# Kernel tuning notes

Measured on AMD Instinct MI355X. Metric: run time of the kernel, lower is better.

Reference implementation:

```python
import jax, jax.numpy as jnp
import numpy as np

# Config (matches init_kwargs)
B, T, N = 32, 512, 1024
FT, FS = 16, 32                 # max_time_F, max_space_F
NCH = FT * FS                   # n_channels = 512
MULT = 2
DIN = NCH * MULT                # input_dim = 1024
H = 1024                        # hidden_size
NCLS = 1                        # n_cls_tokens
NP = (T // FT) * (N // FS)      # n_patches = 1024
SCALE = float(H) ** 0.5         # config.scale is None -> hidden_size**0.5


def setup_inputs() -> dict:
    key = jax.random.key(0)
    k0, k1, k2, k3 = jax.random.split(key, 4)
    s = 0.02
    return {
        "spikes": jax.random.normal(k0, (B, T, N), dtype=jnp.float32),
        "W_embed": jax.random.normal(k1, (DIN, NCH), dtype=jnp.float32) * s,
        "b_embed": jnp.zeros((DIN,), dtype=jnp.float32),
        "cls_tokens": jnp.zeros((1, NCLS, DIN), dtype=jnp.float32),
        "W_proj": jax.random.normal(k2, (H, DIN), dtype=jnp.float32) * s,
        "b_proj": jnp.zeros((H,), dtype=jnp.float32),
        "pos_table": jax.random.normal(k3, (NP + NCLS, H), dtype=jnp.float32) * s,
    }


def reference(spikes, W_embed, b_embed, cls_tokens, W_proj, b_proj, pos_table):
    Bsz = spikes.shape[0]
    # Patchify: replaces the double python loop with one reshape/transpose.
    # [B,T,N] -> [B, T/FT, FT, N/FS, FS] -> [B, T/FT, N/FS, FT, FS] -> [B, NP, NCH]
    # flatten order (time-major within patch) matches torch's .flatten(1) on [B,FT,FS].
    patches = spikes.reshape(Bsz, T // FT, FT, N // FS, FS)
    patches = patches.transpose(0, 1, 3, 2, 4).reshape(Bsz, NP, NCH)
    # embed_spikes (linear)
    x = jnp.einsum("bpc,dc->bpd", patches, W_embed) + b_embed
    # prepend cls tokens
    cls = jnp.broadcast_to(cls_tokens, (Bsz, NCLS, DIN))
    x = jnp.concatenate([cls, x], axis=1)
    # act * scale, then projection
    x = jax.nn.gelu(x, approximate=False) * SCALE
    x = jnp.einsum("bpd,hd->bph", x, W_proj) + b_proj
    # positional embedding: stamps are arange, so direct table add
    stamp = jnp.broadcast_to(
        jnp.arange(NP + NCLS, dtype=jnp.int32)[None, :], (Bsz, NP + NCLS)
    )
    mask = jnp.ones((Bsz, NP + NCLS), dtype=jnp.int32)
    x = x + pos_table[None, :, :]
    # dropout p=0.0 -> identity
    return (x, mask, stamp)
```

## Files before the change

kernel.cpp:

```cpp
#include <hip/hip_runtime.h>
#include <stdint.h>


typedef __attribute__((ext_vector_type(8))) short bf16x8;
typedef __attribute__((ext_vector_type(4))) float f32x4;

__device__ __forceinline__ unsigned short f2bf(float f) {
  union { float f; unsigned u; } v; v.f = f;
  const unsigned u = v.u;
  return (unsigned short)((u + 0x7fffu + ((u >> 16) & 1u)) >> 16);
}

__device__ __forceinline__ float gelu_exact(float x) {
  return 0.5f * x * (1.0f + erff(x * 0.70710678118654752440f));
}

__device__ __forceinline__ void gl_lds16(const unsigned short* g, unsigned short* l) {
  __builtin_amdgcn_global_load_lds(
      (const __attribute__((address_space(1))) unsigned int*)g,
      (__attribute__((address_space(3))) unsigned int*)l, 16, 0, 0);
}


__global__ void cast_f32_bf16(const float* __restrict__ src,
                              unsigned short* __restrict__ dst, int n) {
  const int i = blockIdx.x * 256 + threadIdx.x;
  if (i < n) dst[i] = f2bf(src[i]);
}

__global__ void patchify(const float* __restrict__ spikes,
                         unsigned short* __restrict__ P) {
  const int idx = blockIdx.x * 256 + threadIdx.x;
  const int m = idx >> 7;
  const int c = (idx & 127) << 2;
  const int b = m >> 10, p = m & 1023;
  const int pt = p >> 5, ps = p & 31;
  const int ft = c >> 5, fs = c & 31;
  const float4 v = *(const float4*)(spikes +
      (size_t)(((b << 9) + pt * 16 + ft) << 10) + ps * 32 + fs);
  ushort4 o;
  o.x = f2bf(v.x); o.y = f2bf(v.y); o.z = f2bf(v.z); o.w = f2bf(v.w);
  *(ushort4*)(P + (size_t)m * 512 + c) = o;
}

__global__ void g0_and_pad(const float* __restrict__ cls,
                           unsigned short* __restrict__ G) {
  const int i = blockIdx.x * 256 + threadIdx.x;
  G[(size_t)32800 * 1024 + i] = 0;
  if (i < 1024) {
    const unsigned short bv = f2bf(gelu_exact(cls[i]) * 32.0f);
    for (int b = 0; b < 32; ++b) G[(size_t)(b * 1025) * 1024 + i] = bv;
  }
}

__global__ void mask_stamp(float* __restrict__ out) {
  const int i = blockIdx.x * 256 + threadIdx.x;
  if (i < 32800) {
    out[33587200 + i] = 1.0f;
    out[33587200 + 32800 + i] = (float)(i % 1025);
  }
}

template <int K, bool GELU_EPI, int ROWBLKS>
__global__ __launch_bounds__(256) void gemm_bt(
    const unsigned short* __restrict__ A, const unsigned short* __restrict__ B,
    const float* __restrict__ bias, unsigned short* __restrict__ Cg,
    float* __restrict__ Cf, const float* __restrict__ pos, int Mvalid) {
  __shared__ __align__(16) unsigned short lsA[128 * 64];
  __shared__ __align__(16) unsigned short lsB[128 * 64];
  const int tid = threadIdx.x;
  const int lane = tid & 63;
  const int w = tid >> 6;
  const int quad = lane >> 4;
  const int l16 = lane & 15;

  const int L = blockIdx.x;
  const int xcd = L & 7;
  const int j = L >> 3;
  int rowBlk, colBlk;
  if (ROWBLKS > 256 && j >= 256) { rowBlk = 256; colBlk = xcd; }
  else { rowBlk = xcd * 32 + (j >> 3); colBlk = j & 7; }
  const int rowStart = rowBlk * 128;
  const int colStart = colBlk * 128;
  const int wm = (w >> 1) * 64;
  const int wn = (w & 1) * 64;

  f32x4 acc[4][4];
  const f32x4 z = {0.f, 0.f, 0.f, 0.f};
#pragma unroll
  for (int i = 0; i < 4; ++i)
#pragma unroll
    for (int j2 = 0; j2 < 4; ++j2) acc[i][j2] = z;

  const int g0 = w * 256 + lane;

  for (int k0 = 0; k0 < K; k0 += 64) {
    __syncthreads();
#pragma unroll
    for (int s = 0; s < 4; ++s) {
      const int g = g0 + s * 64;
      const int r = g >> 3;
      const int slot = g & 7;
      const int kc = (slot ^ (r & 7)) * 8;
      gl_lds16(A + (size_t)(rowStart + r) * K + (k0 + kc), lsA + r * 64 + slot * 8);
      gl_lds16(B + (size_t)(colStart + r) * K + (k0 + kc), lsB + r * 64 + slot * 8);
    }
    __syncthreads();
#pragma unroll
    for (int kk = 0; kk < 64; kk += 32) {
      bf16x8 af[4], bfr[4];
      const int kcb = (kk >> 3) + quad;
#pragma unroll
      for (int i = 0; i < 4; ++i) {
        const int r = wm + i * 16 + l16;
        af[i] = *(const bf16x8*)(lsA + r * 64 + (kcb ^ (r & 7)) * 8);
      }
#pragma unroll
      for (int j2 = 0; j2 < 4; ++j2) {
        const int r = wn + j2 * 16 + l16;
        bfr[j2] = *(const bf16x8*)(lsB + r * 64 + (kcb ^ (r & 7)) * 8);
      }
#pragma unroll
      for (int i = 0; i < 4; ++i)
#pragma unroll
        for (int j2 = 0; j2 < 4; ++j2)
          acc[i][j2] = __builtin_amdgcn_mfma_f32_16x16x32_bf16(af[i], bfr[j2],
                                                               acc[i][j2], 0, 0, 0);
    }
  }

#pragma unroll
  for (int i = 0; i < 4; ++i) {
    const int rb = rowStart + wm + i * 16 + quad * 4;
#pragma unroll
    for (int j2 = 0; j2 < 4; ++j2) {
      const int gc = colStart + wn + j2 * 16 + l16;
      const float bv = bias[gc];
#pragma unroll
      for (int r = 0; r < 4; ++r) {
        const int row = rb + r;
        float v = acc[i][j2][r] + bv;
        if (GELU_EPI) {
          v = gelu_exact(v) * 32.0f;
          const int grow = row + (row >> 10) + 1;
          Cg[(size_t)grow * 1024 + gc] = f2bf(v);
        } else {
          if (row < Mvalid) {
            const int p = row % 1025;
            Cf[(size_t)row * 1024 + gc] = v + pos[(size_t)p * 1024 + gc];
          }
        }
      }
    }
  }
}


extern "C" void kernel_launch(void* const* d_in, const int* in_sizes, int n_in,
                              void* d_out, int out_size, void* d_ws, size_t ws_size,
                              hipStream_t stream) {
  const float* spikes  = (const float*)d_in[0];
  const float* W_embed = (const float*)d_in[1];
  const float* b_embed = (const float*)d_in[2];
  const float* cls     = (const float*)d_in[3];
  const float* W_proj  = (const float*)d_in[4];
  const float* b_proj  = (const float*)d_in[5];
  const float* pos     = (const float*)d_in[6];
  float* out = (float*)d_out;

  char* ws = (char*)d_ws;
  unsigned short* P  = (unsigned short*)(ws);
  unsigned short* G  = (unsigned short*)(ws + 33554432);
  unsigned short* WE = (unsigned short*)(ws + 100925440);
  unsigned short* WP = (unsigned short*)(ws + 101974016);

  hipLaunchKernelGGL(cast_f32_bf16, dim3(2048), dim3(256), 0, stream, W_embed, WE, 524288);
  hipLaunchKernelGGL(cast_f32_bf16, dim3(4096), dim3(256), 0, stream, W_proj, WP, 1048576);
  hipLaunchKernelGGL(patchify, dim3(16384), dim3(256), 0, stream, spikes, P);
  hipLaunchKernelGGL(g0_and_pad, dim3(384), dim3(256), 0, stream, cls, G);
  hipLaunchKernelGGL(mask_stamp, dim3(129), dim3(256), 0, stream, out);

  hipLaunchKernelGGL((gemm_bt<512, true, 256>), dim3(2048), dim3(256), 0, stream,
                     P, WE, b_embed, G, (float*)nullptr, (const float*)nullptr, 0);
  hipLaunchKernelGGL((gemm_bt<1024, false, 257>), dim3(2056), dim3(256), 0, stream,
                     G, WP, b_proj, (unsigned short*)nullptr, out, pos, 32800);
}
```

Measured before the change: 428.5 us.

## Use 256x256 tiles with double-buffered LDS and staged async prefetch in GEMMs

Reworks both bf16 GEMMs to 512-thread workgroups computing 256x256 tiles, with double-buffered LDS. The next K-tile is prefetched in four staged chunks interleaved with MFMA phases, using explicit vmcnt waits and barriers instead of full syncthreads. It also raises MFMA priority with setprio and remaps workgroups across XCDs. The aim is to hide global-to-LDS latency and raise arithmetic intensity, at the cost of heavy register pressure from 128 accumulators, 128KB of LDS, and fragile hand-managed wait counts.

```diff
diff --git a/kernel.cpp b/kernel.cpp
--- a/kernel.cpp
+++ b/kernel.cpp
@@ -4,6 +4,9 @@
 
 typedef __attribute__((ext_vector_type(8))) short bf16x8;
 typedef __attribute__((ext_vector_type(4))) float f32x4;
+
+#define VMCNT(n) asm volatile("s_waitcnt vmcnt(" #n ")" ::: "memory")
+#define CFENCE() asm volatile("" ::: "memory")
 
 __device__ __forceinline__ unsigned short f2bf(float f) {
   union { float f; unsigned u; } v; v.f = f;
@@ -61,85 +64,186 @@
   }
 }
 
-template <int K, bool GELU_EPI, int ROWBLKS>
-__global__ __launch_bounds__(256) void gemm_bt(
+
+__device__ __forceinline__ void stageA_chunk(const unsigned short* __restrict__ A,
+    int K, int rowStart, int rmax, unsigned short* lds, int k0, int m0, int lane,
+    int hi) {
+#pragma unroll
+  for (int l = 0; l < 2; ++l) {
+    const int m = m0 + l;
+    const int g = ((m & 8) ? (1024 + ((m & 7) << 6)) : (m << 6)) + hi + lane;
+    const int r = g >> 3, slot = g & 7;
+    const int kc = (slot ^ (r & 7)) << 3;
+    int rg = rowStart + r;
+    if (rg > rmax) rg = rmax;
+    gl_lds16(A + (size_t)rg * K + (k0 + kc), lds + g * 8);
+  }
+}
+
+__device__ __forceinline__ void stageB_chunk(const unsigned short* __restrict__ B,
+    int K, int colStart, unsigned short* lds, int k0, int m0, int lane, int hi) {
+#pragma unroll
+  for (int l = 0; l < 2; ++l) {
+    const int m = m0 + l;
+    const int g = ((m >> 2) << 9) + ((m & 3) << 6) + hi + lane;
+    const int r = g >> 3, slot = g & 7;
+    const int kc = (slot ^ (r & 7)) << 3;
+    gl_lds16(B + (size_t)(colStart + r) * K + (k0 + kc), lds + g * 8);
+  }
+}
+
+template <int K, bool GELU_EPI>
+__global__ __launch_bounds__(512, 2) void gemm_bt(
     const unsigned short* __restrict__ A, const unsigned short* __restrict__ B,
     const float* __restrict__ bias, unsigned short* __restrict__ Cg,
-    float* __restrict__ Cf, const float* __restrict__ pos, int Mvalid) {
-  __shared__ __align__(16) unsigned short lsA[128 * 64];
-  __shared__ __align__(16) unsigned short lsB[128 * 64];
+    float* __restrict__ Cf, const float* __restrict__ pos,
+    int Mvalid, int rmax, int nRowBlk) {
+  __shared__ __align__(16) unsigned short lsA[2][16384];
+  __shared__ __align__(16) unsigned short lsB[2][16384];
+  constexpr int NT = K / 64;
+
   const int tid = threadIdx.x;
   const int lane = tid & 63;
   const int w = tid >> 6;
   const int quad = lane >> 4;
   const int l16 = lane & 15;
-
-  const int L = blockIdx.x;
-  const int xcd = L & 7;
-  const int j = L >> 3;
-  int rowBlk, colBlk;
-  if (ROWBLKS > 256 && j >= 256) { rowBlk = 256; colBlk = xcd; }
-  else { rowBlk = xcd * 32 + (j >> 3); colBlk = j & 7; }
-  const int rowStart = rowBlk * 128;
-  const int colStart = colBlk * 128;
-  const int wm = (w >> 1) * 64;
-  const int wn = (w & 1) * 64;
-
-  f32x4 acc[4][4];
+  const int wm = (w >> 2) * 128;
+  const int wn = (w & 3) * 64;
+  const int m0 = w * 2;
+
+  const int nwg = nRowBlk * 4;
+  const int q = nwg >> 3, rr = nwg & 7;
+  const int xcd = blockIdx.x & 7, jj = blockIdx.x >> 3;
+  const int wgid =
+      (xcd < rr ? xcd * (q + 1) : rr * (q + 1) + (xcd - rr) * q) + jj;
+  const int rowStart = (wgid >> 2) << 8;
+  const int colStart = (wgid & 3) << 8;
+
+  f32x4 acc[8][4];
   const f32x4 z = {0.f, 0.f, 0.f, 0.f};
 #pragma unroll
-  for (int i = 0; i < 4; ++i)
-#pragma unroll
-    for (int j2 = 0; j2 < 4; ++j2) acc[i][j2] = z;
-
-  const int g0 = w * 256 + lane;
-
-  for (int k0 = 0; k0 < K; k0 += 64) {
-    __syncthreads();
-#pragma unroll
-    for (int s = 0; s < 4; ++s) {
-      const int g = g0 + s * 64;
-      const int r = g >> 3;
-      const int slot = g & 7;
-      const int kc = (slot ^ (r & 7)) * 8;
-      gl_lds16(A + (size_t)(rowStart + r) * K + (k0 + kc), lsA + r * 64 + slot * 8);
-      gl_lds16(B + (size_t)(colStart + r) * K + (k0 + kc), lsB + r * 64 + slot * 8);
-    }
-    __syncthreads();
-#pragma unroll
-    for (int kk = 0; kk < 64; kk += 32) {
-      bf16x8 af[4], bfr[4];
-      const int kcb = (kk >> 3) + quad;
-#pragma unroll
-      for (int i = 0; i < 4; ++i) {
-        const int r = wm + i * 16 + l16;
-        af[i] = *(const bf16x8*)(lsA + r * 64 + (kcb ^ (r & 7)) * 8);
-      }
-#pragma unroll
-      for (int j2 = 0; j2 < 4; ++j2) {
-        const int r = wn + j2 * 16 + l16;
-        bfr[j2] = *(const bf16x8*)(lsB + r * 64 + (kcb ^ (r & 7)) * 8);
-      }
-#pragma unroll
-      for (int i = 0; i < 4; ++i)
-#pragma unroll
-        for (int j2 = 0; j2 < 4; ++j2)
-          acc[i][j2] = __builtin_amdgcn_mfma_f32_16x16x32_bf16(af[i], bfr[j2],
-                                                               acc[i][j2], 0, 0, 0);
-    }
-  }
-
-#pragma unroll
-  for (int i = 0; i < 4; ++i) {
+  for (int i = 0; i < 8; ++i)
+#pragma unroll
+    for (int j = 0; j < 4; ++j) acc[i][j] = z;
+
+  stageA_chunk(A, K, rowStart, rmax, lsA[0], 0, m0, lane, 0);
+  stageB_chunk(B, K, colStart, lsB[0], 0, m0, lane, 0);
+  stageB_chunk(B, K, colStart, lsB[0], 0, m0, lane, 256);
+  stageA_chunk(A, K, rowStart, rmax, lsA[0], 0, m0, lane, 512);
+
+  const int aoff = (wm + l16) << 6;
+  const int boff = (wn + l16) << 6;
+  const int sl0 = (quad ^ (l16 & 7)) << 3;
+  const int sl1 = ((4 + quad) ^ (l16 & 7)) << 3;
+
+  for (int t = 0; t < NT; ++t) {
+    const int cur = t & 1;
+    const unsigned short* cA = lsA[cur];
+    const unsigned short* cB = lsB[cur];
+    unsigned short* nA = lsA[cur ^ 1];
+    unsigned short* nB = lsB[cur ^ 1];
+    const int kn = (t + 1) << 6;
+    const bool pf = (t + 1 < NT);
+
+    bf16x8 a0[4][2], a1[4][2], b0[2][2], b1[2][2];
+
+    if (pf) {
+      stageA_chunk(A, K, rowStart, rmax, nA, kn, m0, lane, 0);
+      VMCNT(6);
+    } else {
+      VMCNT(4);
+    }
+    __builtin_amdgcn_s_barrier();
+    CFENCE();
+#pragma unroll
+    for (int i = 0; i < 4; ++i) {
+      a0[i][0] = *(const bf16x8*)(cA + aoff + i * 1024 + sl0);
+      a0[i][1] = *(const bf16x8*)(cA + aoff + i * 1024 + sl1);
+    }
+#pragma unroll
+    for (int j = 0; j < 2; ++j) {
+      b0[j][0] = *(const bf16x8*)(cB + boff + j * 1024 + sl0);
+      b0[j][1] = *(const bf16x8*)(cB + boff + j * 1024 + sl1);
+    }
+    __builtin_amdgcn_s_setprio(1);
+#pragma unroll
+    for (int i = 0; i < 4; ++i)
+#pragma unroll
+      for (int j = 0; j < 2; ++j) {
+        acc[i][j] = __builtin_amdgcn_mfma_f32_16x16x32_bf16(a0[i][0], b0[j][0], acc[i][j], 0, 0, 0);
+        acc[i][j] = __builtin_amdgcn_mfma_f32_16x16x32_bf16(a0[i][1], b0[j][1], acc[i][j], 0, 0, 0);
+      }
+    __builtin_amdgcn_s_setprio(0);
+
+    if (pf) {
+      stageB_chunk(B, K, colStart, nB, kn, m0, lane, 0);
+      VMCNT(6);
+    } else {
+      VMCNT(2);
+    }
+    __builtin_amdgcn_s_barrier();
+    CFENCE();
+#pragma unroll
+    for (int j = 0; j < 2; ++j) {
+      b1[j][0] = *(const bf16x8*)(cB + boff + (j + 2) * 1024 + sl0);
+      b1[j][1] = *(const bf16x8*)(cB + boff + (j + 2) * 1024 + sl1);
+    }
+    __builtin_amdgcn_s_setprio(1);
+#pragma unroll
+    for (int i = 0; i < 4; ++i)
+#pragma unroll
+      for (int j = 0; j < 2; ++j) {
+        acc[i][j + 2] = __builtin_amdgcn_mfma_f32_16x16x32_bf16(a0[i][0], b1[j][0], acc[i][j + 2], 0, 0, 0);
+        acc[i][j + 2] = __builtin_amdgcn_mfma_f32_16x16x32_bf16(a0[i][1], b1[j][1], acc[i][j + 2], 0, 0, 0);
+      }
+    __builtin_amdgcn_s_setprio(0);
+
+    if (pf) {
+      stageB_chunk(B, K, colStart, nB, kn, m0, lane, 256);
+      VMCNT(6);
+    } else {
+      VMCNT(0);
+    }
+    __builtin_amdgcn_s_barrier();
+    CFENCE();
+#pragma unroll
+    for (int i = 0; i < 4; ++i) {
+      a1[i][0] = *(const bf16x8*)(cA + aoff + (i + 4) * 1024 + sl0);
+      a1[i][1] = *(const bf16x8*)(cA + aoff + (i + 4) * 1024 + sl1);
+    }
+    __builtin_amdgcn_s_setprio(1);
+#pragma unroll
+    for (int i = 0; i < 4; ++i)
+#pragma unroll
+      for (int j = 0; j < 2; ++j) {
+        acc[i + 4][j] = __builtin_amdgcn_mfma_f32_16x16x32_bf16(a1[i][0], b0[j][0], acc[i + 4][j], 0, 0, 0);
+        acc[i + 4][j] = __builtin_amdgcn_mfma_f32_16x16x32_bf16(a1[i][1], b0[j][1], acc[i + 4][j], 0, 0, 0);
+      }
+    __builtin_amdgcn_s_setprio(0);
+
+    if (pf) stageA_chunk(A, K, rowStart, rmax, nA, kn, m0, lane, 512);
+    __builtin_amdgcn_s_setprio(1);
+#pragma unroll
+    for (int i = 0; i < 4; ++i)
+#pragma unroll
+      for (int j = 0; j < 2; ++j) {
+        acc[i + 4][j + 2] = __builtin_amdgcn_mfma_f32_16x16x32_bf16(a1[i][0], b1[j][0], acc[i + 4][j + 2], 0, 0, 0);
+        acc[i + 4][j + 2] = __builtin_amdgcn_mfma_f32_16x16x32_bf16(a1[i][1], b1[j][1], acc[i + 4][j + 2], 0, 0, 0);
+      }
+    __builtin_amdgcn_s_setprio(0);
+  }
+
+#pragma unroll
+  for (int i = 0; i < 8; ++i) {
     const int rb = rowStart + wm + i * 16 + quad * 4;
 #pragma unroll
-    for (int j2 = 0; j2 < 4; ++j2) {
-      const int gc = colStart + wn + j2 * 16 + l16;
+    for (int j = 0; j < 4; ++j) {
+      const int gc = colStart + wn + j * 16 + l16;
       const float bv = bias[gc];
 #pragma unroll
       for (int r = 0; r < 4; ++r) {
         const int row = rb + r;
-        float v = acc[i][j2][r] + bv;
+        float v = acc[i][j][r] + bv;
         if (GELU_EPI) {
           v = gelu_exact(v) * 32.0f;
           const int grow = row + (row >> 10) + 1;
@@ -180,8 +284,10 @@
   hipLaunchKernelGGL(g0_and_pad, dim3(384), dim3(256), 0, stream, cls, G);
   hipLaunchKernelGGL(mask_stamp, dim3(129), dim3(256), 0, stream, out);
 
-  hipLaunchKernelGGL((gemm_bt<512, true, 256>), dim3(2048), dim3(256), 0, stream,
-                     P, WE, b_embed, G, (float*)nullptr, (const float*)nullptr, 0);
-  hipLaunchKernelGGL((gemm_bt<1024, false, 257>), dim3(2056), dim3(256), 0, stream,
-                     G, WP, b_proj, (unsigned short*)nullptr, out, pos, 32800);
-}
+  hipLaunchKernelGGL((gemm_bt<512, true>), dim3(512), dim3(512), 0, stream,
+                     P, WE, b_embed, G, (float*)nullptr, (const float*)nullptr,
+                     0, 32767, 128);
+  hipLaunchKernelGGL((gemm_bt<1024, false>), dim3(516), dim3(512), 0, stream,
+                     G, WP, b_proj, (unsigned short*)nullptr, out, pos,
+                     32800, 32895, 129);
+}
```

Measured after the change: 471.5 us. +10.0%, slower.

## Double-buffer LDS tiles in bf16 GEMM to overlap loads with MFMA

Applied to the files above, without the earlier changes.

Gives the GEMM kernel two LDS buffers per operand and prefetches the next K-tile with global_load_lds while the current tile feeds the MFMAs. An explicit vmcnt wait plus raw s_barrier replaces the two __syncthreads per iteration, so the next tile's loads stay in flight during compute. This is meant to hide global-memory latency in the K loop. In exchange, LDS use per block doubles to 64KB, which may reduce how many blocks fit on a CU.

```diff
diff --git a/kernel.cpp b/kernel.cpp
--- a/kernel.cpp
+++ b/kernel.cpp
@@ -4,6 +4,9 @@
 
 typedef __attribute__((ext_vector_type(8))) short bf16x8;
 typedef __attribute__((ext_vector_type(4))) float f32x4;
+
+#define VMCNT(n) asm volatile("s_waitcnt vmcnt(" #n ")" ::: "memory")
+#define CFENCE() asm volatile("" ::: "memory")
 
 __device__ __forceinline__ unsigned short f2bf(float f) {
   union { float f; unsigned u; } v; v.f = f;
@@ -61,13 +64,30 @@
   }
 }
 
+__device__ __forceinline__ void stage_tile(
+    const unsigned short* __restrict__ A, const unsigned short* __restrict__ B,
+    int K, int rowStart, int colStart, int k0, int g0,
+    unsigned short* la, unsigned short* lb) {
+#pragma unroll
+  for (int s = 0; s < 4; ++s) {
+    const int g = g0 + s * 64;
+    const int r = g >> 3;
+    const int slot = g & 7;
+    const int kc = (slot ^ (r & 7)) << 3;
+    gl_lds16(A + (size_t)(rowStart + r) * K + (k0 + kc), la + r * 64 + slot * 8);
+    gl_lds16(B + (size_t)(colStart + r) * K + (k0 + kc), lb + r * 64 + slot * 8);
+  }
+}
+
 template <int K, bool GELU_EPI, int ROWBLKS>
 __global__ __launch_bounds__(256) void gemm_bt(
     const unsigned short* __restrict__ A, const unsigned short* __restrict__ B,
     const float* __restrict__ bias, unsigned short* __restrict__ Cg,
     float* __restrict__ Cf, const float* __restrict__ pos, int Mvalid) {
-  __shared__ __align__(16) unsigned short lsA[128 * 64];
-  __shared__ __align__(16) unsigned short lsB[128 * 64];
+  __shared__ __align__(16) unsigned short lsA[2][128 * 64];
+  __shared__ __align__(16) unsigned short lsB[2][128 * 64];
+  constexpr int NT = K / 64;
+
   const int tid = threadIdx.x;
   const int lane = tid & 63;
   const int w = tid >> 6;
@@ -94,18 +114,22 @@
 
   const int g0 = w * 256 + lane;
 
-  for (int k0 = 0; k0 < K; k0 += 64) {
-    __syncthreads();
-#pragma unroll
-    for (int s = 0; s < 4; ++s) {
-      const int g = g0 + s * 64;
-      const int r = g >> 3;
-      const int slot = g & 7;
-      const int kc = (slot ^ (r & 7)) * 8;
-      gl_lds16(A + (size_t)(rowStart + r) * K + (k0 + kc), lsA + r * 64 + slot * 8);
-      gl_lds16(B + (size_t)(colStart + r) * K + (k0 + kc), lsB + r * 64 + slot * 8);
+  stage_tile(A, B, K, rowStart, colStart, 0, g0, lsA[0], lsB[0]);
+
+  for (int t = 0; t < NT; ++t) {
+    const int cur = t & 1;
+    if (t + 1 < NT) {
+      stage_tile(A, B, K, rowStart, colStart, (t + 1) * 64, g0,
+                 lsA[cur ^ 1], lsB[cur ^ 1]);
+      VMCNT(8);
+    } else {
+      VMCNT(0);
     }
-    __syncthreads();
+    __builtin_amdgcn_s_barrier();
+    CFENCE();
+
+    const unsigned short* cA = lsA[cur];
+    const unsigned short* cB = lsB[cur];
 #pragma unroll
     for (int kk = 0; kk < 64; kk += 32) {
       bf16x8 af[4], bfr[4];
@@ -113,12 +137,12 @@
 #pragma unroll
       for (int i = 0; i < 4; ++i) {
         const int r = wm + i * 16 + l16;
-        af[i] = *(const bf16x8*)(lsA + r * 64 + (kcb ^ (r & 7)) * 8);
+        af[i] = *(const bf16x8*)(cA + r * 64 + ((kcb ^ (r & 7)) << 3));
       }
 #pragma unroll
       for (int j2 = 0; j2 < 4; ++j2) {
         const int r = wn + j2 * 16 + l16;
-        bfr[j2] = *(const bf16x8*)(lsB + r * 64 + (kcb ^ (r & 7)) * 8);
+        bfr[j2] = *(const bf16x8*)(cB + r * 64 + ((kcb ^ (r & 7)) << 3));
       }
 #pragma unroll
       for (int i = 0; i < 4; ++i)
@@ -127,6 +151,10 @@
           acc[i][j2] = __builtin_amdgcn_mfma_f32_16x16x32_bf16(af[i], bfr[j2],
                                                                acc[i][j2], 0, 0, 0);
     }
+
+    CFENCE();
+    __builtin_amdgcn_s_barrier();
+    CFENCE();
   }
 
 #pragma unroll
```

Result: faster. 419.9 us (-2.0%).
